# Optimization experiments

Measured on AMD Instinct MI355X. Metric: run time of the kernel, lower is better.

Reference implementation:

```python
import jax, jax.numpy as jnp
import numpy as np


def gcn_conv(x, src, dst, deg_inv_sqrt, W, b, n_nodes):
    # PyG GCNConv: linear transform first, then normalized aggregation (A_hat = D^-1/2 (A+I) D^-1/2)
    h = x @ W                                   # [N, out]
    norm = deg_inv_sqrt[src] * deg_inv_sqrt[dst]  # [E+N]
    msg = h[src] * norm[:, None]                # gather + scale
    out = jax.ops.segment_sum(msg, dst, num_segments=n_nodes)
    return out + b


def setup_inputs() -> dict:
    key = jax.random.key(0)
    ks = jax.random.split(key, 10)
    N, E, D_in, D_h = 50000, 640000, 128, 64
    x = jax.random.normal(ks[0], (N, D_in), dtype=jnp.float32)
    edge_index = jax.random.randint(ks[1], (2, E), 0, N, dtype=jnp.int64)

    def glorot(k, fan_in, fan_out):
        lim = jnp.sqrt(6.0 / (fan_in + fan_out)).astype(jnp.float32)
        return jax.random.uniform(k, (fan_in, fan_out), jnp.float32, -lim, lim)

    return {
        "x": x,
        "edge_index": edge_index,
        "W1": glorot(ks[2], D_in, D_h), "b1": jnp.zeros((D_h,), jnp.float32),
        "W2": glorot(ks[3], D_h, D_h),  "b2": jnp.zeros((D_h,), jnp.float32),
        "W3": glorot(ks[4], D_h, D_h),  "b3": jnp.zeros((D_h,), jnp.float32),
        "W4": glorot(ks[5], D_h, D_in), "b4": jnp.zeros((D_in,), jnp.float32),
    }


def reference(x, edge_index, W1, b1, W2, b2, W3, b3, W4, b4):
    n = x.shape[0]
    loops = jnp.arange(n, dtype=edge_index.dtype)
    src = jnp.concatenate([edge_index[0], loops])  # A + I self-loops
    dst = jnp.concatenate([edge_index[1], loops])
    deg = jax.ops.segment_sum(jnp.ones_like(dst, dtype=x.dtype), dst, num_segments=n)
    deg_inv_sqrt = jnp.where(deg > 0, jax.lax.rsqrt(deg), 0.0)

    h = jax.nn.relu(gcn_conv(x, src, dst, deg_inv_sqrt, W1, b1, n))
    # dropout is identity in eval mode
    z = jax.nn.relu(gcn_conv(h, src, dst, deg_inv_sqrt, W2, b2, n))
    x_hat = jax.nn.relu(gcn_conv(z, src, dst, deg_inv_sqrt, W3, b3, n))
    x_hat = gcn_conv(x_hat, src, dst, deg_inv_sqrt, W4, b4, n)
    return (x_hat, z)
```

## Files before the change

kernel.cpp:

```cpp
#include <hip/hip_runtime.h>
#include <hip/hip_bf16.h>



__global__ __launch_bounds__(256) void init_k(int* __restrict__ deg, int Npad) {
    int i = blockIdx.x * 256 + threadIdx.x;
    if (i < Npad) deg[i] = 0;
}

__global__ __launch_bounds__(256) void hist_deg(const int* __restrict__ dst,
                                                int* __restrict__ deg, int E) {
    int e = blockIdx.x * 256 + threadIdx.x;
    if (e < E) atomicAdd(&deg[dst[e]], 1);
}

__global__ __launch_bounds__(256) void scan_phase1(const int* __restrict__ deg,
                                                   int* __restrict__ block_sums) {
    int b = blockIdx.x, t = threadIdx.x;
    const int4* p = reinterpret_cast<const int4*>(deg + (size_t)b * 2048);
    int4 a = p[t * 2], c = p[t * 2 + 1];
    int s = a.x + a.y + a.z + a.w + c.x + c.y + c.z + c.w;
#pragma unroll
    for (int off = 32; off; off >>= 1) s += __shfl_down(s, off);
    __shared__ int wsum[4];
    if ((t & 63) == 0) wsum[t >> 6] = s;
    __syncthreads();
    if (t == 0) block_sums[b] = wsum[0] + wsum[1] + wsum[2] + wsum[3];
}

__global__ __launch_bounds__(256) void scan_phase2(const int* __restrict__ block_sums,
                                                   int* __restrict__ block_off,
                                                   int* __restrict__ row_ptr,
                                                   int B, int N) {
    __shared__ int s[256];
    int t = threadIdx.x;
    int v = (t < B) ? block_sums[t] : 0;
    s[t] = v;
    __syncthreads();
#pragma unroll
    for (int off = 1; off < 256; off <<= 1) {
        int u = (t >= off) ? s[t - off] : 0;
        __syncthreads();
        s[t] += u;
        __syncthreads();
    }
    if (t < B) block_off[t] = s[t] - v;
    if (t == 255) row_ptr[N] = s[255];
}

__global__ __launch_bounds__(256) void scan_phase3(const int* __restrict__ deg,
                                                   const int* __restrict__ block_off,
                                                   int* __restrict__ row_ptr,
                                                   float* __restrict__ dis, int N) {
    int b = blockIdx.x, t = threadIdx.x;
    int base = b * 2048 + t * 8;
    const int4* p = reinterpret_cast<const int4*>(deg + base);
    int4 a = p[0], c = p[1];
    int d[8] = {a.x, a.y, a.z, a.w, c.x, c.y, c.z, c.w};
    int pre[8], s = 0;
#pragma unroll
    for (int j = 0; j < 8; ++j) { pre[j] = s; s += d[j]; }
    __shared__ int ls[256];
    ls[t] = s;
    __syncthreads();
#pragma unroll
    for (int off = 1; off < 256; off <<= 1) {
        int u = (t >= off) ? ls[t - off] : 0;
        __syncthreads();
        ls[t] += u;
        __syncthreads();
    }
    int excl = ls[t] - s + block_off[b];
#pragma unroll
    for (int j = 0; j < 8; ++j) {
        int i = base + j;
        if (i < N) {
            row_ptr[i] = excl + pre[j];
            dis[i] = rsqrtf((float)(d[j] + 1));
        }
    }
}

__global__ __launch_bounds__(256) void fill_csr(const int* __restrict__ src,
                                                const int* __restrict__ dst,
                                                const int* __restrict__ row_ptr,
                                                int* __restrict__ deg,
                                                int* __restrict__ csr_src, int E) {
    int e = blockIdx.x * 256 + threadIdx.x;
    if (e < E) {
        int d = dst[e];
        int old = atomicSub(&deg[d], 1);
        csr_src[row_ptr[d] + old - 1] = src[e];
    }
}


__device__ __forceinline__ ushort r16(float f) {
    __hip_bfloat16 h = __float2bfloat16(f);
    return *reinterpret_cast<ushort*>(&h);
}
__device__ __forceinline__ float bf_lo(unsigned u) {
    return __builtin_bit_cast(float, u << 16);
}
__device__ __forceinline__ float bf_hi(unsigned u) {
    return __builtin_bit_cast(float, u & 0xFFFF0000u);
}

__device__ __forceinline__ void gather_pair_u2(const unsigned* __restrict__ G,
                                               const int* __restrict__ csr_src,
                                               int begA, int lenA,
                                               int begB, int lenB, int lane,
                                               float& s0o, float& s1o,
                                               float& s2o, float& s3o) {
    int l32 = lane & 31;
    int idxA = 0, idxB = 0;
    if (lenA > 0) idxA = csr_src[begA + (l32 < lenA ? l32 : lenA - 1)];
    if (lenB > 0) idxB = csr_src[begB + (l32 < lenB ? l32 : lenB - 1)];

    int grp     = lane >> 4;
    int p       = grp & 1;
    int nodeSel = grp >> 1;
    int f       = lane & 15;

    int cA = lenA < 32 ? lenA : 32;
    int cB = lenB < 32 ? lenB : 32;
    int cOwn = nodeSel ? cB : cA;
    int cM = cA > cB ? cA : cB;
    int pM = (cM + 1) >> 1;

    float a0 = 0.f, a1 = 0.f, a2 = 0.f, a3 = 0.f;
    float b0 = 0.f, b1 = 0.f, b2 = 0.f, b3 = 0.f;

    for (int k = 0; k < pM; k += 8) {
        uint2 u[8];
        int ee[8];
#pragma unroll
        for (int i = 0; i < 8; ++i) {
            int e = p + 2 * (k + i);
            ee[i] = e;
            int sA = __shfl(idxA, e);
            int sB = __shfl(idxB, e);
            int s = nodeSel ? sB : sA;
            u[i] = *reinterpret_cast<const uint2*>(G + (unsigned)s * 32u + 2 * f);
        }
#pragma unroll
        for (int i = 0; i < 8; ++i) {
            unsigned ux = (ee[i] < cOwn) ? u[i].x : 0u;
            unsigned uy = (ee[i] < cOwn) ? u[i].y : 0u;
            if (i & 1) {
                b0 += bf_lo(ux); b1 += bf_hi(ux);
                b2 += bf_lo(uy); b3 += bf_hi(uy);
            } else {
                a0 += bf_lo(ux); a1 += bf_hi(ux);
                a2 += bf_lo(uy); a3 += bf_hi(uy);
            }
        }
    }
    int begOwn = nodeSel ? begB : begA;
    int lenOwn = nodeSel ? lenB : lenA;
    for (int e2 = 32 + p; e2 < lenOwn; e2 += 2) {
        int s = csr_src[begOwn + e2];
        uint2 v = *reinterpret_cast<const uint2*>(G + (unsigned)s * 32u + 2 * f);
        a0 += bf_lo(v.x); a1 += bf_hi(v.x);
        a2 += bf_lo(v.y); a3 += bf_hi(v.y);
    }

    float r0 = a0 + b0, r1 = a1 + b1, r2 = a2 + b2, r3 = a3 + b3;
    r0 += __shfl_xor(r0, 16);
    r1 += __shfl_xor(r1, 16);
    r2 += __shfl_xor(r2, 16);
    r3 += __shfl_xor(r3, 16);
    s0o = r0; s1o = r1; s2o = r2; s3o = r3;
}

template <int K, int DOUT>
__global__ __launch_bounds__(256) void gemm_scale(const float* __restrict__ A,
                                                  const float* __restrict__ W,
                                                  const float* __restrict__ dis,
                                                  ushort* __restrict__ G16, int N) {
    constexpr int CG   = DOUT / 4;
    constexpr int RG   = 256 / CG;
    constexpr int ROWS = RG * 4;
    constexpr int LDA  = K + 4;

    __shared__ __align__(16) float a_lds[ROWS * LDA];
    __shared__ __align__(16) float w_lds[K * DOUT];

    int t    = threadIdx.x;
    int row0 = blockIdx.x * ROWS;

    constexpr int WF4 = K * DOUT / 4;
    for (int q = t; q < WF4; q += 256)
        reinterpret_cast<float4*>(w_lds)[q] =
            reinterpret_cast<const float4*>(W)[q];

    constexpr int AF4 = ROWS * K / 4;
    for (int q = t; q < AF4; q += 256) {
        int r  = q / (K / 4);
        int kc = q % (K / 4);
        float4 v = make_float4(0.f, 0.f, 0.f, 0.f);
        int gr = row0 + r;
        if (gr < N)
            v = reinterpret_cast<const float4*>(A + (size_t)gr * K)[kc];
        *reinterpret_cast<float4*>(&a_lds[r * LDA + kc * 4]) = v;
    }
    __syncthreads();

    int c0 = (t % CG) * 4;
    int r0 = (t / CG) * 4;

    float4 acc[4] = {};
#pragma unroll 1
    for (int k = 0; k < K; k += 4) {
        float4 w0 = *reinterpret_cast<const float4*>(&w_lds[(k + 0) * DOUT + c0]);
        float4 w1 = *reinterpret_cast<const float4*>(&w_lds[(k + 1) * DOUT + c0]);
        float4 w2 = *reinterpret_cast<const float4*>(&w_lds[(k + 2) * DOUT + c0]);
        float4 w3 = *reinterpret_cast<const float4*>(&w_lds[(k + 3) * DOUT + c0]);
#pragma unroll
        for (int j = 0; j < 4; ++j) {
            float4 a4 = *reinterpret_cast<const float4*>(&a_lds[(r0 + j) * LDA + k]);
            acc[j].x += a4.x * w0.x + a4.y * w1.x + a4.z * w2.x + a4.w * w3.x;
            acc[j].y += a4.x * w0.y + a4.y * w1.y + a4.z * w2.y + a4.w * w3.y;
            acc[j].z += a4.x * w0.z + a4.y * w1.z + a4.z * w2.z + a4.w * w3.z;
            acc[j].w += a4.x * w0.w + a4.y * w1.w + a4.z * w2.w + a4.w * w3.w;
        }
    }

#pragma unroll
    for (int j = 0; j < 4; ++j) {
        int gr = row0 + r0 + j;
        if (gr < N) {
            float s = dis[gr];
            float4 o = acc[j];
            ushort4 pk;
            pk.x = r16(o.x * s); pk.y = r16(o.y * s);
            pk.z = r16(o.z * s); pk.w = r16(o.w * s);
            *reinterpret_cast<ushort4*>(&G16[(size_t)gr * DOUT + c0]) = pk;
        }
    }
}

template <int K, int DOUT>
__global__ __launch_bounds__(256) void gemm_bias(const float* __restrict__ A,
                                                 const float* __restrict__ W,
                                                 const float* __restrict__ bias,
                                                 float* __restrict__ Out, int N) {
    constexpr int CG   = DOUT / 4;
    constexpr int RG   = 256 / CG;
    constexpr int ROWS = RG * 4;
    constexpr int LDA  = K + 4;

    __shared__ __align__(16) float a_lds[ROWS * LDA];
    __shared__ __align__(16) float w_lds[K * DOUT];

    int t    = threadIdx.x;
    int row0 = blockIdx.x * ROWS;

    constexpr int WF4 = K * DOUT / 4;
    for (int q = t; q < WF4; q += 256)
        reinterpret_cast<float4*>(w_lds)[q] =
            reinterpret_cast<const float4*>(W)[q];

    constexpr int AF4 = ROWS * K / 4;
    for (int q = t; q < AF4; q += 256) {
        int r  = q / (K / 4);
        int kc = q % (K / 4);
        float4 v = make_float4(0.f, 0.f, 0.f, 0.f);
        int gr = row0 + r;
        if (gr < N)
            v = reinterpret_cast<const float4*>(A + (size_t)gr * K)[kc];
        *reinterpret_cast<float4*>(&a_lds[r * LDA + kc * 4]) = v;
    }
    __syncthreads();

    int c0 = (t % CG) * 4;
    int r0 = (t / CG) * 4;

    float4 acc[4] = {};
#pragma unroll 1
    for (int k = 0; k < K; k += 4) {
        float4 w0 = *reinterpret_cast<const float4*>(&w_lds[(k + 0) * DOUT + c0]);
        float4 w1 = *reinterpret_cast<const float4*>(&w_lds[(k + 1) * DOUT + c0]);
        float4 w2 = *reinterpret_cast<const float4*>(&w_lds[(k + 2) * DOUT + c0]);
        float4 w3 = *reinterpret_cast<const float4*>(&w_lds[(k + 3) * DOUT + c0]);
#pragma unroll
        for (int j = 0; j < 4; ++j) {
            float4 a4 = *reinterpret_cast<const float4*>(&a_lds[(r0 + j) * LDA + k]);
            acc[j].x += a4.x * w0.x + a4.y * w1.x + a4.z * w2.x + a4.w * w3.x;
            acc[j].y += a4.x * w0.y + a4.y * w1.y + a4.z * w2.y + a4.w * w3.y;
            acc[j].z += a4.x * w0.z + a4.y * w1.z + a4.z * w2.z + a4.w * w3.z;
            acc[j].w += a4.x * w0.w + a4.y * w1.w + a4.z * w2.w + a4.w * w3.w;
        }
    }

    float4 b4v = *reinterpret_cast<const float4*>(&bias[c0]);
#pragma unroll
    for (int j = 0; j < 4; ++j) {
        int gr = row0 + r0 + j;
        if (gr < N) {
            float4 o = acc[j];
            o.x += b4v.x; o.y += b4v.y; o.z += b4v.z; o.w += b4v.w;
            reinterpret_cast<float4*>(Out + (size_t)gr * DOUT)[c0 / 4] = o;
        }
    }
}

template <bool WRITE_F32>
__global__ __launch_bounds__(256) void agg_gemm_pair(
    const unsigned* __restrict__ G,
    const int* __restrict__ row_ptr,
    const int* __restrict__ csr_src,
    const float* __restrict__ dis,
    const float* __restrict__ bias,
    const float* __restrict__ Wn,
    unsigned* __restrict__ Gout,
    float* __restrict__ Zout,
    int N) {
    __shared__ __align__(16) float w_lds[64 * 64];
    __shared__ __align__(16) float a_buf[4][2][64];

    int t = threadIdx.x;
    for (int q = t; q < 64 * 64 / 4; q += 256)
        reinterpret_cast<float4*>(w_lds)[q] =
            reinterpret_cast<const float4*>(Wn)[q];
    __syncthreads();

    int wave = t >> 6, lane = t & 63;
    int h = lane >> 5, fl = lane & 31;
    int grp = lane >> 4, f = lane & 15;

    int n0 = (blockIdx.x * 4 + wave) * 2;
    if (n0 >= N) return;
    int n1 = n0 + 1;
    bool hasB = (n1 < N);
    int n1c = hasB ? n1 : n0;
    int nn = h ? n1c : n0;

    int begA = row_ptr[n0];
    int endA = row_ptr[n0 + 1];
    int lenA = endA - begA;
    int begB = 0, lenB = 0;
    if (hasB) { begB = endA; lenB = row_ptr[n0 + 2] - endA; }

    float dn0 = dis[n0], dn1 = dis[n1c];
    uint2 us2 = *reinterpret_cast<const uint2*>(G + (size_t)nn * 32 + 2 * f);
    float4 b4 = reinterpret_cast<const float4*>(bias)[f];

    float s0, s1, s2, s3;
    gather_pair_u2(G, csr_src, begA, lenA, begB, lenB, lane, s0, s1, s2, s3);

    float dn = h ? dn1 : dn0;
    float v0 = fmaxf(dn * (s0 + bf_lo(us2.x)) + b4.x, 0.f);
    float v1 = fmaxf(dn * (s1 + bf_hi(us2.x)) + b4.y, 0.f);
    float v2 = fmaxf(dn * (s2 + bf_lo(us2.y)) + b4.z, 0.f);
    float v3 = fmaxf(dn * (s3 + bf_hi(us2.y)) + b4.w, 0.f);

    if ((grp & 1) == 0)
        *reinterpret_cast<float4*>(&a_buf[wave][h][4 * f]) =
            make_float4(v0, v1, v2, v3);
    if (WRITE_F32 && (grp == 0 || (grp == 2 && hasB)))
        *reinterpret_cast<float4*>(Zout + (size_t)nn * 64 + 4 * f) =
            make_float4(v0, v1, v2, v3);

    __builtin_amdgcn_wave_barrier();

    float yA0 = 0.f, yA1 = 0.f, yA2 = 0.f, yA3 = 0.f;
    float yB0 = 0.f, yB1 = 0.f, yB2 = 0.f, yB3 = 0.f;
    for (int k = 0; k < 64; k += 4) {
        float4 a4 = *reinterpret_cast<const float4*>(&a_buf[wave][0][k]);
        float4 c4 = *reinterpret_cast<const float4*>(&a_buf[wave][1][k]);
        float w0 = w_lds[(k + 0) * 64 + lane];
        float w1 = w_lds[(k + 1) * 64 + lane];
        float w2 = w_lds[(k + 2) * 64 + lane];
        float w3 = w_lds[(k + 3) * 64 + lane];
        yA0 += a4.x * w0; yA1 += a4.y * w1; yA2 += a4.z * w2; yA3 += a4.w * w3;
        yB0 += c4.x * w0; yB1 += c4.y * w1; yB2 += c4.z * w2; yB3 += c4.w * w3;
    }
    float yA = (yA0 + yA1) + (yA2 + yA3);
    float yB = (yB0 + yB1) + (yB2 + yB3);

    float l0 = __shfl(yA, 2 * fl), h0 = __shfl(yA, 2 * fl + 1);
    float l1 = __shfl(yB, 2 * fl), h1 = __shfl(yB, 2 * fl + 1);
    float yl = h ? l1 : l0;
    float yh = h ? h1 : h0;
    if (h == 0 || hasB) {
        unsigned pk = (unsigned)r16(dn * yl) | ((unsigned)r16(dn * yh) << 16);
        Gout[(unsigned)nn * 32u + fl] = pk;
    }
}

__global__ __launch_bounds__(256) void aggregate_s3(const unsigned* __restrict__ G,
                                                    const int* __restrict__ row_ptr,
                                                    const int* __restrict__ csr_src,
                                                    const float* __restrict__ dis,
                                                    const float* __restrict__ bias,
                                                    unsigned* __restrict__ Out, int N) {
    int t = threadIdx.x;
    int wave = t >> 6, lane = t & 63;
    int h = lane >> 5;
    int grp = lane >> 4, f = lane & 15;

    int n0 = (blockIdx.x * 4 + wave) * 2;
    if (n0 >= N) return;
    int n1 = n0 + 1;
    bool hasB = (n1 < N);
    int n1c = hasB ? n1 : n0;
    int nn = h ? n1c : n0;

    int begA = row_ptr[n0];
    int endA = row_ptr[n0 + 1];
    int lenA = endA - begA;
    int begB = 0, lenB = 0;
    if (hasB) { begB = endA; lenB = row_ptr[n0 + 2] - endA; }

    float dn0 = dis[n0], dn1 = dis[n1c];
    uint2 us2 = *reinterpret_cast<const uint2*>(G + (size_t)nn * 32 + 2 * f);
    float4 b4 = reinterpret_cast<const float4*>(bias)[f];

    float s0, s1, s2, s3;
    gather_pair_u2(G, csr_src, begA, lenA, begB, lenB, lane, s0, s1, s2, s3);

    float dn = h ? dn1 : dn0;
    float o0 = fmaxf(dn * (s0 + bf_lo(us2.x)) + b4.x, 0.f);
    float o1 = fmaxf(dn * (s1 + bf_hi(us2.x)) + b4.y, 0.f);
    float o2 = fmaxf(dn * (s2 + bf_lo(us2.y)) + b4.z, 0.f);
    float o3 = fmaxf(dn * (s3 + bf_hi(us2.y)) + b4.w, 0.f);

    if (grp == 0 || (grp == 2 && hasB)) {
        uint2 pk2;
        pk2.x = (unsigned)r16(dn * o0) | ((unsigned)r16(dn * o1) << 16);
        pk2.y = (unsigned)r16(dn * o2) | ((unsigned)r16(dn * o3) << 16);
        *reinterpret_cast<uint2*>(Out + (size_t)nn * 32 + 2 * f) = pk2;
    }
}

__global__ __launch_bounds__(256) void aggregate_t(const unsigned* __restrict__ G,
                                                   const int* __restrict__ row_ptr,
                                                   const int* __restrict__ csr_src,
                                                   const float* __restrict__ dis,
                                                   float* __restrict__ Out, int N) {
    int t = threadIdx.x;
    int wave = t >> 6, lane = t & 63;
    int h = lane >> 5;
    int grp = lane >> 4, f = lane & 15;

    int n0 = (blockIdx.x * 4 + wave) * 2;
    if (n0 >= N) return;
    int n1 = n0 + 1;
    bool hasB = (n1 < N);
    int n1c = hasB ? n1 : n0;
    int nn = h ? n1c : n0;

    int begA = row_ptr[n0];
    int endA = row_ptr[n0 + 1];
    int lenA = endA - begA;
    int begB = 0, lenB = 0;
    if (hasB) { begB = endA; lenB = row_ptr[n0 + 2] - endA; }

    float dn0 = dis[n0], dn1 = dis[n1c];
    uint2 us2 = *reinterpret_cast<const uint2*>(G + (size_t)nn * 32 + 2 * f);

    float s0, s1, s2, s3;
    gather_pair_u2(G, csr_src, begA, lenA, begB, lenB, lane, s0, s1, s2, s3);

    float dn = h ? dn1 : dn0;
    if (grp == 0 || (grp == 2 && hasB))
        *reinterpret_cast<float4*>(Out + (size_t)nn * 64 + 4 * f) =
            make_float4(dn * (s0 + bf_lo(us2.x)), dn * (s1 + bf_hi(us2.x)),
                        dn * (s2 + bf_lo(us2.y)), dn * (s3 + bf_hi(us2.y)));
}


extern "C" void kernel_launch(void* const* d_in, const int* in_sizes, int n_in,
                              void* d_out, int out_size, void* d_ws, size_t ws_size,
                              hipStream_t stream) {
    const float* x     = (const float*)d_in[0];
    const int*   edges = (const int*)d_in[1];
    const float* W1 = (const float*)d_in[2];
    const float* b1 = (const float*)d_in[3];
    const float* W2 = (const float*)d_in[4];
    const float* b2 = (const float*)d_in[5];
    const float* W3 = (const float*)d_in[6];
    const float* b3 = (const float*)d_in[7];
    const float* W4 = (const float*)d_in[8];
    const float* b4 = (const float*)d_in[9];

    const int DIN = 128, DH = 64;
    int N = in_sizes[0] / DIN;
    int E = in_sizes[1] / 2;

    const int* e_src = edges;
    const int* e_dst = edges + E;

    float* out   = (float*)d_out;
    float* x_hat = out;
    float* z     = out + (size_t)N * DIN;

    int B    = (N + 2047) / 2048;
    int Npad = B * 2048;

    char*  ws  = (char*)d_ws;
    size_t woff = 0;
    auto carve = [&](size_t bytes) {
        void* p = ws + woff;
        woff = (woff + bytes + 255) & ~(size_t)255;
        return p;
    };
    float*    dis        = (float*)   carve((size_t)N * 4);
    int*      deg        = (int*)     carve((size_t)Npad * 4);
    int*      row_ptr    = (int*)     carve((size_t)(N + 1) * 4);
    int*      csr_src    = (int*)     carve((size_t)E * 4);
    int*      block_sums = (int*)     carve((size_t)B * 4);
    int*      block_off  = (int*)     carve((size_t)B * 4);
    unsigned* gA         = (unsigned*)carve((size_t)N * DH * 2);
    unsigned* gB         = (unsigned*)carve((size_t)N * DH * 2);
    float*    t          = (float*)   carve((size_t)N * DH * 4);
    (void)ws_size;

    int nb_e = (E + 255) / 256;
    int nb_p = (N + 7) / 8;

    init_k<<<(Npad + 255) / 256, 256, 0, stream>>>(deg, Npad);
    hist_deg<<<nb_e, 256, 0, stream>>>(e_dst, deg, E);
    scan_phase1<<<B, 256, 0, stream>>>(deg, block_sums);
    scan_phase2<<<1, 256, 0, stream>>>(block_sums, block_off, row_ptr, B, N);
    scan_phase3<<<B, 256, 0, stream>>>(deg, block_off, row_ptr, dis, N);
    fill_csr<<<nb_e, 256, 0, stream>>>(e_src, e_dst, row_ptr, deg, csr_src, E);

    gemm_scale<128, 64><<<(N + 63) / 64, 256, 0, stream>>>(
        x, W1, dis, (ushort*)gA, N);

    agg_gemm_pair<false><<<nb_p, 256, 0, stream>>>(
        gA, row_ptr, csr_src, dis, b1, W2, gB, nullptr, N);

    agg_gemm_pair<true><<<nb_p, 256, 0, stream>>>(
        gB, row_ptr, csr_src, dis, b2, W3, gA, z, N);

    aggregate_s3<<<nb_p, 256, 0, stream>>>(
        gA, row_ptr, csr_src, dis, b3, gB, N);

    aggregate_t<<<nb_p, 256, 0, stream>>>(
        gB, row_ptr, csr_src, dis, t, N);
    gemm_bias<64, 128><<<(N + 31) / 32, 256, 0, stream>>>(t, W4, b4, x_hat, N);
}
```

Measured before the change: 286.1 us.

## Fuse final aggregation with W4 GEMM and bias into one kernel

Replaces the last aggregate kernel plus separate gemm_bias with one fused kernel. Each wave aggregates two nodes, stages their 64-wide results in LDS, then multiplies by W4 (held in 32KB LDS) and writes the 128-wide output with bias. This removes the fp32 intermediate round trip through global memory and one launch. The cost is loading W4 into LDS per 512-thread block and a per-wave GEMM that reads W4 from LDS, which may limit occupancy.

```diff
diff --git a/kernel.cpp b/kernel.cpp
--- a/kernel.cpp
+++ b/kernel.cpp
@@ -236,71 +236,6 @@
             pk.x = r16(o.x * s); pk.y = r16(o.y * s);
             pk.z = r16(o.z * s); pk.w = r16(o.w * s);
             *reinterpret_cast<ushort4*>(&G16[(size_t)gr * DOUT + c0]) = pk;
-        }
-    }
-}
-
-template <int K, int DOUT>
-__global__ __launch_bounds__(256) void gemm_bias(const float* __restrict__ A,
-                                                 const float* __restrict__ W,
-                                                 const float* __restrict__ bias,
-                                                 float* __restrict__ Out, int N) {
-    constexpr int CG   = DOUT / 4;
-    constexpr int RG   = 256 / CG;
-    constexpr int ROWS = RG * 4;
-    constexpr int LDA  = K + 4;
-
-    __shared__ __align__(16) float a_lds[ROWS * LDA];
-    __shared__ __align__(16) float w_lds[K * DOUT];
-
-    int t    = threadIdx.x;
-    int row0 = blockIdx.x * ROWS;
-
-    constexpr int WF4 = K * DOUT / 4;
-    for (int q = t; q < WF4; q += 256)
-        reinterpret_cast<float4*>(w_lds)[q] =
-            reinterpret_cast<const float4*>(W)[q];
-
-    constexpr int AF4 = ROWS * K / 4;
-    for (int q = t; q < AF4; q += 256) {
-        int r  = q / (K / 4);
-        int kc = q % (K / 4);
-        float4 v = make_float4(0.f, 0.f, 0.f, 0.f);
-        int gr = row0 + r;
-        if (gr < N)
-            v = reinterpret_cast<const float4*>(A + (size_t)gr * K)[kc];
-        *reinterpret_cast<float4*>(&a_lds[r * LDA + kc * 4]) = v;
-    }
-    __syncthreads();
-
-    int c0 = (t % CG) * 4;
-    int r0 = (t / CG) * 4;
-
-    float4 acc[4] = {};
-#pragma unroll 1
-    for (int k = 0; k < K; k += 4) {
-        float4 w0 = *reinterpret_cast<const float4*>(&w_lds[(k + 0) * DOUT + c0]);
-        float4 w1 = *reinterpret_cast<const float4*>(&w_lds[(k + 1) * DOUT + c0]);
-        float4 w2 = *reinterpret_cast<const float4*>(&w_lds[(k + 2) * DOUT + c0]);
-        float4 w3 = *reinterpret_cast<const float4*>(&w_lds[(k + 3) * DOUT + c0]);
-#pragma unroll
-        for (int j = 0; j < 4; ++j) {
-            float4 a4 = *reinterpret_cast<const float4*>(&a_lds[(r0 + j) * LDA + k]);
-            acc[j].x += a4.x * w0.x + a4.y * w1.x + a4.z * w2.x + a4.w * w3.x;
-            acc[j].y += a4.x * w0.y + a4.y * w1.y + a4.z * w2.y + a4.w * w3.y;
-            acc[j].z += a4.x * w0.z + a4.y * w1.z + a4.z * w2.z + a4.w * w3.z;
-            acc[j].w += a4.x * w0.w + a4.y * w1.w + a4.z * w2.w + a4.w * w3.w;
-        }
-    }
-
-    float4 b4v = *reinterpret_cast<const float4*>(&bias[c0]);
-#pragma unroll
-    for (int j = 0; j < 4; ++j) {
-        int gr = row0 + r0 + j;
-        if (gr < N) {
-            float4 o = acc[j];
-            o.x += b4v.x; o.y += b4v.y; o.z += b4v.z; o.w += b4v.w;
-            reinterpret_cast<float4*>(Out + (size_t)gr * DOUT)[c0 / 4] = o;
         }
     }
 }
@@ -434,17 +369,29 @@
     }
 }
 
-__global__ __launch_bounds__(256) void aggregate_t(const unsigned* __restrict__ G,
-                                                   const int* __restrict__ row_ptr,
-                                                   const int* __restrict__ csr_src,
-                                                   const float* __restrict__ dis,
-                                                   float* __restrict__ Out, int N) {
+__global__ __launch_bounds__(512) void agg_w4_fused(
+    const unsigned* __restrict__ G,
+    const int* __restrict__ row_ptr,
+    const int* __restrict__ csr_src,
+    const float* __restrict__ dis,
+    const float* __restrict__ bias,
+    const float* __restrict__ W4,
+    float* __restrict__ Out,
+    int N) {
+    __shared__ __align__(16) float w_lds[64 * 128];
+    __shared__ __align__(16) float a_buf[8][2][64];
+
     int t = threadIdx.x;
+    for (int q = t; q < 64 * 128 / 4; q += 512)
+        reinterpret_cast<float4*>(w_lds)[q] =
+            reinterpret_cast<const float4*>(W4)[q];
+    __syncthreads();
+
     int wave = t >> 6, lane = t & 63;
     int h = lane >> 5;
     int grp = lane >> 4, f = lane & 15;
 
-    int n0 = (blockIdx.x * 4 + wave) * 2;
+    int n0 = (blockIdx.x * 8 + wave) * 2;
     if (n0 >= N) return;
     int n1 = n0 + 1;
     bool hasB = (n1 < N);
@@ -464,10 +411,43 @@
     gather_pair_u2(G, csr_src, begA, lenA, begB, lenB, lane, s0, s1, s2, s3);
 
     float dn = h ? dn1 : dn0;
-    if (grp == 0 || (grp == 2 && hasB))
-        *reinterpret_cast<float4*>(Out + (size_t)nn * 64 + 4 * f) =
-            make_float4(dn * (s0 + bf_lo(us2.x)), dn * (s1 + bf_hi(us2.x)),
-                        dn * (s2 + bf_lo(us2.y)), dn * (s3 + bf_hi(us2.y)));
+    float t0 = dn * (s0 + bf_lo(us2.x));
+    float t1 = dn * (s1 + bf_hi(us2.x));
+    float t2 = dn * (s2 + bf_lo(us2.y));
+    float t3 = dn * (s3 + bf_hi(us2.y));
+
+    if ((grp & 1) == 0)
+        *reinterpret_cast<float4*>(&a_buf[wave][h][4 * f]) =
+            make_float4(t0, t1, t2, t3);
+
+    __builtin_amdgcn_wave_barrier();
+
+    float yA0 = 0.f, yA1 = 0.f, yB0 = 0.f, yB1 = 0.f;
+    for (int k = 0; k < 64; k += 4) {
+        float4 a4 = *reinterpret_cast<const float4*>(&a_buf[wave][0][k]);
+        float4 c4 = *reinterpret_cast<const float4*>(&a_buf[wave][1][k]);
+        float w00 = w_lds[(k + 0) * 128 + lane];
+        float w01 = w_lds[(k + 0) * 128 + lane + 64];
+        float w10 = w_lds[(k + 1) * 128 + lane];
+        float w11 = w_lds[(k + 1) * 128 + lane + 64];
+        float w20 = w_lds[(k + 2) * 128 + lane];
+        float w21 = w_lds[(k + 2) * 128 + lane + 64];
+        float w30 = w_lds[(k + 3) * 128 + lane];
+        float w31 = w_lds[(k + 3) * 128 + lane + 64];
+        yA0 += a4.x * w00 + a4.y * w10 + a4.z * w20 + a4.w * w30;
+        yA1 += a4.x * w01 + a4.y * w11 + a4.z * w21 + a4.w * w31;
+        yB0 += c4.x * w00 + c4.y * w10 + c4.z * w20 + c4.w * w30;
+        yB1 += c4.x * w01 + c4.y * w11 + c4.z * w21 + c4.w * w31;
+    }
+
+    float bA = bias[lane];
+    float bB = bias[lane + 64];
+    Out[(size_t)n0 * 128 + lane]      = yA0 + bA;
+    Out[(size_t)n0 * 128 + lane + 64] = yA1 + bB;
+    if (hasB) {
+        Out[(size_t)n1 * 128 + lane]      = yB0 + bA;
+        Out[(size_t)n1 * 128 + lane + 64] = yB1 + bB;
+    }
 }
 
 
@@ -514,11 +494,11 @@
     int*      block_off  = (int*)     carve((size_t)B * 4);
     unsigned* gA         = (unsigned*)carve((size_t)N * DH * 2);
     unsigned* gB         = (unsigned*)carve((size_t)N * DH * 2);
-    float*    t          = (float*)   carve((size_t)N * DH * 4);
     (void)ws_size;
 
     int nb_e = (E + 255) / 256;
     int nb_p = (N + 7) / 8;
+    int nb_4 = (N + 15) / 16;
 
     init_k<<<(Npad + 255) / 256, 256, 0, stream>>>(deg, Npad);
     hist_deg<<<nb_e, 256, 0, stream>>>(e_dst, deg, E);
@@ -539,7 +519,6 @@
     aggregate_s3<<<nb_p, 256, 0, stream>>>(
         gA, row_ptr, csr_src, dis, b3, gB, N);
 
-    aggregate_t<<<nb_p, 256, 0, stream>>>(
-        gB, row_ptr, csr_src, dis, t, N);
-    gemm_bias<64, 128><<<(N + 31) / 32, 256, 0, stream>>>(t, W4, b4, x_hat, N);
-}
+    agg_w4_fused<<<nb_4, 512, 0, stream>>>(
+        gB, row_ptr, csr_src, dis, b4, W4, x_hat, N);
+}
```

New measurement: 309.2 us. 8.1% more time.
